# Performance work log

Hardware: AMD Instinct MI355X
Metric: run time of the kernel (lower is better)

Reference implementation:

```python
import jax, jax.numpy as jnp
import numpy as np

B = 4194304  # batch of timesteps
F = 16       # number of Fourier frequencies


def setup_inputs() -> dict:
    key = jax.random.key(0)
    k_t, k_f, k_s, k_c = jax.random.split(key, 4)
    t = jax.random.normal(k_t, (B,), dtype=jnp.float32)
    freqs = jax.random.uniform(k_f, (F,), dtype=jnp.float32)
    offset_fixed = jnp.float32(0.5)
    sin_coeff = jax.random.normal(k_s, (F,), dtype=jnp.float32)
    cos_coeff = jax.random.normal(k_c, (F,), dtype=jnp.float32)
    return {"t": t, "freqs": freqs, "offset_fixed": offset_fixed,
            "sin_coeff": sin_coeff, "cos_coeff": cos_coeff}


def reference(t, freqs, offset_fixed, sin_coeff, cos_coeff):
    # arg: [B, F] = outer product of timesteps and frequencies
    arg = t[:, None] * freqs[None, :]
    ts = jnp.sin(arg) @ sin_coeff  # [B]
    tc = jnp.cos(arg) @ cos_coeff  # [B]
    frange = jnp.maximum(
        jnp.float32(1.0),
        jnp.sum(jnp.abs(sin_coeff)) + jnp.sum(jnp.abs(cos_coeff)) + jnp.float32(1e-8),
    )
    return (offset_fixed + ts + tc) / frange
```

## Files before the change

kernel.cpp:

```cpp
#include <hip/hip_runtime.h>
#include <math.h>

#define NF 16
#define B_ELEMS 4194304

#define INV_2PI 0.15915494309189535f

__global__ void fourier_setup_kernel(const float* __restrict__ freqs,
                                     const float* __restrict__ offp,
                                     const float* __restrict__ sc,
                                     const float* __restrict__ cc,
                                     float* __restrict__ ws) {
    int lane = threadIdx.x;
    float s = 0.f, c = 0.f, fq = 0.f;
    if (lane < NF) { s = sc[lane]; c = cc[lane]; fq = freqs[lane]; }
    float absum = fabsf(s) + fabsf(c);
    #pragma unroll
    for (int off = 1; off < 64; off <<= 1)
        absum += __shfl_xor(absum, off, 64);
    float frange = fmaxf(1.0f, absum + 1e-8f);
    float inv = 1.0f / frange;
    if (lane < NF) {
        float R   = sqrtf(s * s + c * c);
        float phi = atan2f(c, s);
        ws[lane]          = fq * INV_2PI;
        ws[NF + lane]     = phi * INV_2PI;
        ws[2 * NF + lane] = R * inv;
    }
    if (lane == 0) ws[3 * NF] = offp[0] * inv;
}

__global__ __launch_bounds__(256) void fourier_main_kernel(
        const float* __restrict__ t,
        const float* __restrict__ ws,
        float* __restrict__ out,
        int n4) {
    float f2[NF], p2[NF], Rs[NF];
    #pragma unroll
    for (int k = 0; k < NF; ++k) {
        f2[k] = ws[k];
        p2[k] = ws[NF + k];
        Rs[k] = ws[2 * NF + k];
    }
    float off = ws[3 * NF];

    int idx    = blockIdx.x * blockDim.x + threadIdx.x;
    int stride = gridDim.x * blockDim.x;
    const float4* __restrict__ t4 = (const float4*)t;
    float4* __restrict__ o4       = (float4*)out;

    for (int i = idx; i < n4; i += stride) {
        float4 tv = t4[i];
        float tt[4] = {tv.x, tv.y, tv.z, tv.w};
        float acc[4];
        #pragma unroll
        for (int j = 0; j < 4; ++j) acc[j] = off;
        #pragma unroll
        for (int k = 0; k < NF; ++k) {
            #pragma unroll
            for (int j = 0; j < 4; ++j) {
                float r = fmaf(tt[j], f2[k], p2[k]);
                acc[j] = fmaf(Rs[k], __builtin_amdgcn_sinf(r), acc[j]);
            }
        }
        float4 ov;
        ov.x = acc[0]; ov.y = acc[1]; ov.z = acc[2]; ov.w = acc[3];
        o4[i] = ov;
    }
}

extern "C" void kernel_launch(void* const* d_in, const int* in_sizes, int n_in,
                              void* d_out, int out_size, void* d_ws, size_t ws_size,
                              hipStream_t stream) {
    const float* t     = (const float*)d_in[0];
    const float* freqs = (const float*)d_in[1];
    const float* offp  = (const float*)d_in[2];
    const float* sc    = (const float*)d_in[3];
    const float* cc    = (const float*)d_in[4];
    float* out = (float*)d_out;
    float* ws  = (float*)d_ws;

    fourier_setup_kernel<<<1, 64, 0, stream>>>(freqs, offp, sc, cc, ws);

    int n4 = out_size / 4;
    int block = 256;
    int grid  = 2048;
    fourier_main_kernel<<<grid, block, 0, stream>>>(t, ws, out, n4);
}
```

Before: 82.26 us.

## Fuse coefficient setup into main kernel and enlarge grid

Drops the separate single-block setup kernel. Each block now computes the amplitude/phase coefficients into shared memory itself, which removes one launch and the dependency between two kernels. Every block redoes the small setup work, including an atan2f, and must pass a __syncthreads before its main loop. The grid is also raised from 2048 to up to 4096 blocks.

```diff
diff --git a/kernel.cpp b/kernel.cpp
--- a/kernel.cpp
+++ b/kernel.cpp
@@ -2,52 +2,53 @@
 #include <math.h>
 
 #define NF 16
-#define B_ELEMS 4194304
-
 #define INV_2PI 0.15915494309189535f
 
-__global__ void fourier_setup_kernel(const float* __restrict__ freqs,
-                                     const float* __restrict__ offp,
-                                     const float* __restrict__ sc,
-                                     const float* __restrict__ cc,
-                                     float* __restrict__ ws) {
-    int lane = threadIdx.x;
-    float s = 0.f, c = 0.f, fq = 0.f;
-    if (lane < NF) { s = sc[lane]; c = cc[lane]; fq = freqs[lane]; }
-    float absum = fabsf(s) + fabsf(c);
-    #pragma unroll
-    for (int off = 1; off < 64; off <<= 1)
-        absum += __shfl_xor(absum, off, 64);
-    float frange = fmaxf(1.0f, absum + 1e-8f);
-    float inv = 1.0f / frange;
-    if (lane < NF) {
-        float R   = sqrtf(s * s + c * c);
-        float phi = atan2f(c, s);
-        ws[lane]          = fq * INV_2PI;
-        ws[NF + lane]     = phi * INV_2PI;
-        ws[2 * NF + lane] = R * inv;
-    }
-    if (lane == 0) ws[3 * NF] = offp[0] * inv;
-}
-
-__global__ __launch_bounds__(256) void fourier_main_kernel(
+__global__ __launch_bounds__(256) void fourier_fused_kernel(
         const float* __restrict__ t,
-        const float* __restrict__ ws,
+        const float* __restrict__ freqs,
+        const float* __restrict__ offp,
+        const float* __restrict__ sc,
+        const float* __restrict__ cc,
         float* __restrict__ out,
         int n4) {
+    __shared__ float sh[3 * NF + 1];
+    const int tid = threadIdx.x;
+
+    if (tid < 64) {
+        float s = 0.f, c = 0.f, fq = 0.f;
+        if (tid < NF) { s = sc[tid]; c = cc[tid]; fq = freqs[tid]; }
+        float absum = fabsf(s) + fabsf(c);
+        #pragma unroll
+        for (int off = 1; off < NF; off <<= 1)
+            absum += __shfl_xor(absum, off, 64);
+        if (tid < NF) {
+            float frange = fmaxf(1.0f, absum + 1e-8f);
+            float inv = 1.0f / frange;
+            float R   = sqrtf(s * s + c * c);
+            float phi = atan2f(c, s);
+            sh[tid]          = fq * INV_2PI;
+            sh[NF + tid]     = phi * INV_2PI;
+            sh[2 * NF + tid] = R * inv;
+            if (tid == 0) sh[3 * NF] = offp[0] * inv;
+        }
+    }
+    __syncthreads();
+
     float f2[NF], p2[NF], Rs[NF];
     #pragma unroll
     for (int k = 0; k < NF; ++k) {
-        f2[k] = ws[k];
-        p2[k] = ws[NF + k];
-        Rs[k] = ws[2 * NF + k];
+        f2[k] = sh[k];
+        p2[k] = sh[NF + k];
+        Rs[k] = sh[2 * NF + k];
     }
-    float off = ws[3 * NF];
+    const float off = sh[3 * NF];
 
-    int idx    = blockIdx.x * blockDim.x + threadIdx.x;
-    int stride = gridDim.x * blockDim.x;
     const float4* __restrict__ t4 = (const float4*)t;
     float4* __restrict__ o4       = (float4*)out;
+
+    int idx    = blockIdx.x * blockDim.x + tid;
+    int stride = gridDim.x * blockDim.x;
 
     for (int i = idx; i < n4; i += stride) {
         float4 tv = t4[i];
@@ -78,12 +79,11 @@
     const float* sc    = (const float*)d_in[3];
     const float* cc    = (const float*)d_in[4];
     float* out = (float*)d_out;
-    float* ws  = (float*)d_ws;
-
-    fourier_setup_kernel<<<1, 64, 0, stream>>>(freqs, offp, sc, cc, ws);
+    (void)d_ws; (void)ws_size;
 
     int n4 = out_size / 4;
     int block = 256;
-    int grid  = 2048;
-    fourier_main_kernel<<<grid, block, 0, stream>>>(t, ws, out, n4);
+    int grid  = (n4 + block - 1) / block;
+    if (grid > 4096) grid = 4096;
+    fourier_fused_kernel<<<grid, block, 0, stream>>>(t, freqs, offp, sc, cc, out, n4);
 }
```

After: 83.17 us. About the same (+1.1%).
